# Kernel tuning notes

Hardware: AMD Instinct MI355X
Metric: run time of the kernel (lower is better)

The kernel has to match this reference:

```python
import jax, jax.numpy as jnp
import numpy as np


def conv2d(x, w, b, pad):
    y = jax.lax.conv_general_dilated(x, w, (1, 1), [(pad, pad), (pad, pad)],
                                     dimension_numbers=('NCHW', 'OIHW', 'NCHW'))
    return y + b[None, :, None, None]


def setup_inputs() -> dict:
    key = jax.random.key(0)
    ks = jax.random.split(key, 24)
    bs, C, OC, K = 2, 64, 3, 3
    hi = wi = 96
    ho = wo = 192

    def _w(k, o, i, kh, kw):
        return jax.random.normal(k, (o, i, kh, kw), jnp.float32) / np.float32(np.sqrt(i * kh * kw))

    inp = {
        'x': jax.random.normal(ks[0], (bs, C, hi, wi), jnp.float32),
        'poseMap': jax.random.normal(ks[1], (1, 3, ho, wo), jnp.float32),
        'interMapY': jax.random.randint(ks[2], (ho, wo), 0, hi, jnp.int32),
        'interMapX': jax.random.randint(ks[3], (ho, wo), 0, wi, jnp.int32),
        # sigmaconv: 3x3 convs 64->64->64->2
        'sig_w1': _w(ks[4], 64, 64, 3, 3), 'sig_b1': jnp.zeros((64,), jnp.float32),
        'sig_w2': _w(ks[5], 64, 64, 3, 3), 'sig_b2': jnp.zeros((64,), jnp.float32),
        'sig_w3': _w(ks[6], 2, 64, 3, 3), 'sig_b3': jnp.zeros((2,), jnp.float32),
        # dwconv: 1x1 convs 3->64->256->C*K*K
        'dw_w1': _w(ks[7], 64, 3, 1, 1), 'dw_b1': jnp.zeros((64,), jnp.float32),
        'dw_w2': _w(ks[8], 256, 64, 1, 1), 'dw_b2': jnp.zeros((256,), jnp.float32),
        'dw_w3': _w(ks[9], C * K * K, 256, 1, 1), 'dw_b3': jnp.zeros((C * K * K,), jnp.float32),
        # pwconv: 1x1 convs 3->64->256->C*OC
        'pw_w1': _w(ks[10], 64, 3, 1, 1), 'pw_b1': jnp.zeros((64,), jnp.float32),
        'pw_w2': _w(ks[11], 256, 64, 1, 1), 'pw_b2': jnp.zeros((256,), jnp.float32),
        'pw_w3': _w(ks[12], C * OC, 256, 1, 1), 'pw_b3': jnp.zeros((C * OC,), jnp.float32),
    }
    return inp


def reference(x, poseMap, interMapY, interMapX,
              sig_w1, sig_b1, sig_w2, sig_b2, sig_w3, sig_b3,
              dw_w1, dw_b1, dw_w2, dw_b2, dw_w3, dw_b3,
              pw_w1, pw_b1, pw_w2, pw_b2, pw_w3, pw_b3):
    C, K, OC = 64, 3, 3
    bs, _, hi, wi = x.shape
    ho, wo = poseMap.shape[2], poseMap.shape[3]
    pad = K // 2

    p = jax.lax.stop_gradient(poseMap)  # original detaches poseMap
    # kernel-predict branches (1x1 conv MLPs over position map)
    dw = conv2d(jax.nn.relu(conv2d(jax.nn.relu(conv2d(p, dw_w1, dw_b1, 0)), dw_w2, dw_b2, 0)), dw_w3, dw_b3, 0)
    dw = dw.reshape(1, C, K * K, ho, wo)
    pw = conv2d(jax.nn.relu(conv2d(jax.nn.relu(conv2d(p, pw_w1, pw_b1, 0)), pw_w2, pw_b2, 0)), pw_w3, pw_b3, 0)
    pw = pw.reshape(C, OC, ho, wo)

    # unfold(x, K, padding=K//2): [bs, C, K*K, hi, wi], kernel taps row-major
    xp = jnp.pad(x, ((0, 0), (0, 0), (pad, pad), (pad, pad)))
    h = jnp.stack([xp[:, :, dy:dy + hi, dx:dx + wi]
                   for dy in range(K) for dx in range(K)], axis=2)
    # irregular spatial gather to HR grid: [bs, C, K*K, ho, wo]
    h = h[:, :, :, interMapY, interMapX]

    mean = jnp.sum(h * jax.nn.softmax(dw, axis=2), axis=2)  # [bs, C, ho, wo]
    sigma = conv2d(jax.nn.relu(conv2d(jax.nn.relu(conv2d(mean, sig_w1, sig_b1, 1)), sig_w2, sig_b2, 1)), sig_w3, sig_b3, 1)
    sigmad = sigma[:, 0:1, None, :, :]
    sigmar = sigma[:, 1:2, None, :, :]
    bw = sigmad * dw + sigmar * jnp.abs(h - mean[:, :, None, :, :])
    xa = jnp.sum(h * jax.nn.softmax(bw, axis=2), axis=2)  # [bs, C, ho, wo]
    out = jnp.einsum('bchw,cohw->bohw', xa, pw)  # [bs, OC, ho, wo]
    return out
```

## Files before the change

kernel.cpp:

```cpp
#include <hip/hip_runtime.h>
#include <hip/hip_bf16.h>

#define NPIX 36864

typedef __attribute__((ext_vector_type(8))) short short8;
typedef __attribute__((ext_vector_type(4))) short short4v;
typedef __attribute__((ext_vector_type(4))) float float4v;

__device__ inline unsigned short f2b(float x) {
    return __builtin_bit_cast(unsigned short, __float2bfloat16(x));
}
__device__ inline float b2f(unsigned short h) {
    return __uint_as_float(((unsigned int)h) << 16);
}

#define WB_TOTAL 312320
#define XCAST_N  1179648
__global__ __launch_bounds__(256) void prep_all(
    const float* __restrict__ dw2, const float* __restrict__ dw3,
    const float* __restrict__ pw2, const float* __restrict__ pw3,
    const float* __restrict__ sw1, const float* __restrict__ sw2,
    const float* __restrict__ sw3, unsigned short* __restrict__ wb,
    const float* __restrict__ x, unsigned short* __restrict__ xb)
{
    int i = blockIdx.x * 256 + threadIdx.x;
    if (i >= WB_TOTAL) {
        int j = i - WB_TOTAL;
        if (j < XCAST_N) xb[j] = f2b(x[j]);
        return;
    }
    unsigned short v;
    if (i < 16384)        v = f2b(dw2[i]);
    else if (i < 32768)   v = f2b(pw2[i - 16384]);
    else if (i < 180224)  v = f2b(dw3[i - 32768]);
    else if (i < 229376)  v = f2b(pw3[i - 180224]);
    else if (i < 266240) { int j = i - 229376; int t = j / 4096, r = j % 4096, oc = r / 64, ic = r % 64;
                           v = f2b(sw1[(oc * 64 + ic) * 9 + t]); }
    else if (i < 303104) { int j = i - 266240; int t = j / 4096, r = j % 4096, oc = r / 64, ic = r % 64;
                           v = f2b(sw2[(oc * 64 + ic) * 9 + t]); }
    else                 { int j = i - 303104; int t = j / 1024, r = j % 1024, oc = r / 64, ic = r % 64;
                           v = (oc < 2) ? f2b(sw3[(oc * 64 + ic) * 9 + t]) : (unsigned short)0; }
    wb[i] = v;
}

__global__ __launch_bounds__(256) void mlp_fused(
    const float* __restrict__ pose,
    const float* __restrict__ w1A, const float* __restrict__ b1A,
    const float* __restrict__ w1B, const float* __restrict__ b1B,
    const unsigned short* __restrict__ w2A, const unsigned short* __restrict__ w2B,
    const float* __restrict__ b2A, const float* __restrict__ b2B,
    const unsigned short* __restrict__ w33,
    const float* __restrict__ b3A, const float* __restrict__ b3B,
    unsigned short* __restrict__ outA, unsigned short* __restrict__ outB)
{
    __shared__ unsigned short sh[16384 + 4096];
    unsigned short* h2s = sh;
    unsigned short* Ts  = sh;
    unsigned short* h1s = sh + 16384;
    const int tid = threadIdx.x;
    const int u = blockIdx.y;
    const int chain = (u == 3) ? 1 : 0;
    const int px0 = blockIdx.x * 64;
    const int w = tid >> 6, l = tid & 63;
    const int ln = l & 15, lkg = l >> 4, lk = lkg * 8;
    const float* w1 = chain ? w1B : w1A;
    const float* b1 = chain ? b1B : b1A;
    const unsigned short* w2 = chain ? w2B : w2A;
    const float* b2 = chain ? b2B : b2A;
    {
        int px = px0 + l;
        float p0 = pose[px], p1 = pose[NPIX + px], p2 = pose[2 * NPIX + px];
        short8 s0, s1;
        #pragma unroll
        for (int j = 0; j < 16; ++j) {
            int oc = w * 16 + j;
            float v = b1[oc] + w1[oc * 3] * p0 + w1[oc * 3 + 1] * p1 + w1[oc * 3 + 2] * p2;
            unsigned short uv = f2b(fmaxf(v, 0.f));
            if (j < 8) s0[j] = (short)uv; else s1[j - 8] = (short)uv;
        }
        *(short8*)&h1s[(w * 2 + 0) * 512 + l * 8] = s0;
        *(short8*)&h1s[(w * 2 + 1) * 512 + l * 8] = s1;
    }
    __syncthreads();
    {
        short8 b0v[4], b1v[4];
        #pragma unroll
        for (int nt = 0; nt < 4; ++nt) {
            b0v[nt] = *(const short8*)&h1s[(lkg    ) * 512 + (nt * 16 + ln) * 8];
            b1v[nt] = *(const short8*)&h1s[(4 + lkg) * 512 + (nt * 16 + ln) * 8];
        }
        float4v acc[4][4] = {};
        #pragma unroll
        for (int mt = 0; mt < 4; ++mt) {
            int ocr = w * 64 + mt * 16 + ln;
            short8 a0 = *(const short8*)&w2[(size_t)ocr * 64 + lk];
            short8 a1 = *(const short8*)&w2[(size_t)ocr * 64 + 32 + lk];
            #pragma unroll
            for (int nt = 0; nt < 4; ++nt) {
                acc[mt][nt] = __builtin_amdgcn_mfma_f32_16x16x32_bf16(a0, b0v[nt], acc[mt][nt], 0, 0, 0);
                acc[mt][nt] = __builtin_amdgcn_mfma_f32_16x16x32_bf16(a1, b1v[nt], acc[mt][nt], 0, 0, 0);
            }
        }
        #pragma unroll
        for (int mt = 0; mt < 4; ++mt) {
            int ocb = w * 64 + mt * 16 + lkg * 4;
            int chk = ocb >> 3, pos = (lkg & 1) * 4;
            float bv0 = b2[ocb + 0], bv1 = b2[ocb + 1], bv2 = b2[ocb + 2], bv3 = b2[ocb + 3];
            #pragma unroll
            for (int nt = 0; nt < 4; ++nt) {
                int pxl = nt * 16 + ln;
                short4v pk;
                pk[0] = (short)f2b(fmaxf(acc[mt][nt][0] + bv0, 0.f));
                pk[1] = (short)f2b(fmaxf(acc[mt][nt][1] + bv1, 0.f));
                pk[2] = (short)f2b(fmaxf(acc[mt][nt][2] + bv2, 0.f));
                pk[3] = (short)f2b(fmaxf(acc[mt][nt][3] + bv3, 0.f));
                *(short4v*)&h2s[chk * 512 + pxl * 8 + pos] = pk;
            }
        }
    }
    __syncthreads();
    const int rowbase = chain ? 576 : u * 192;
    const int obase   = chain ? 0 : u * 192;
    const float* b3 = chain ? b3B : b3A;
    unsigned short* outp = chain ? outB : outA;
    float4v acc[3][4] = {};
    const int r0 = rowbase + w * 48 + ln;
    #pragma unroll
    for (int kc = 0; kc < 8; ++kc) {
        short8 a0 = *(const short8*)&w33[(size_t)(r0 +  0) * 256 + kc * 32 + lk];
        short8 a1 = *(const short8*)&w33[(size_t)(r0 + 16) * 256 + kc * 32 + lk];
        short8 a2 = *(const short8*)&w33[(size_t)(r0 + 32) * 256 + kc * 32 + lk];
        #pragma unroll
        for (int nt = 0; nt < 4; ++nt) {
            short8 b = *(const short8*)&h2s[(kc * 4 + lkg) * 512 + (nt * 16 + ln) * 8];
            acc[0][nt] = __builtin_amdgcn_mfma_f32_16x16x32_bf16(a0, b, acc[0][nt], 0, 0, 0);
            acc[1][nt] = __builtin_amdgcn_mfma_f32_16x16x32_bf16(a1, b, acc[1][nt], 0, 0, 0);
            acc[2][nt] = __builtin_amdgcn_mfma_f32_16x16x32_bf16(a2, b, acc[2][nt], 0, 0, 0);
        }
    }
    __syncthreads();
    #pragma unroll
    for (int mt = 0; mt < 3; ++mt) {
        const int tr = w * 48 + mt * 16 + lkg * 4;
        #pragma unroll
        for (int r = 0; r < 4; ++r) {
            float bv = b3[obase + tr + r];
            #pragma unroll
            for (int nt = 0; nt < 4; ++nt)
                Ts[(tr + r) * 72 + nt * 16 + ln] = f2b(acc[mt][nt][r] + bv);
        }
    }
    __syncthreads();
    for (int i = tid; i < 1536; i += 256) {
        int row = i >> 3, pc = (i & 7) * 8;
        *(short8*)&outp[(size_t)(obase + row) * NPIX + px0 + pc] = *(const short8*)&Ts[row * 72 + pc];
    }
}

template<int MT>
__global__ __launch_bounds__(256) void conv3x3_mfma(
    const unsigned short* __restrict__ act, const unsigned short* __restrict__ wgt,
    const float* __restrict__ bias, unsigned short* __restrict__ out,
    int relu)
{
    constexpr int SP = 72;
    constexpr int OCP = MT * 16;
    __shared__ unsigned short Bs[4 * 66 * SP];
    const int tid = threadIdx.x;
    int bx = blockIdx.x;
    const int xt = bx % 3; bx /= 3;
    const int yg = bx % 96; const int b = bx / 96;
    const int y0 = yg * 2;
    const int x0 = xt * 64;
    const size_t actb = (size_t)b * NPIX * 64;
    const int w = tid >> 6, l = tid & 63;
    const int ln = l & 15, lkg = l >> 4, lk = lkg * 8;
    const int mt = (MT == 4) ? w : 0;
    short8 Wr[9][2];
    #pragma unroll
    for (int t = 0; t < 9; ++t)
        #pragma unroll
        for (int hh = 0; hh < 2; ++hh)
            Wr[t][hh] = *(const short8*)&wgt[((size_t)t * OCP + mt * 16 + ln) * 64 + hh * 32 + lk];
    for (int s = tid; s < 264; s += 256) {
        int r = s / 66, i = s % 66;
        int yy = y0 + r - 1, xx = x0 + i - 1;
        unsigned short* dst = &Bs[(r * 66 + i) * SP];
        if (yy >= 0 && yy < 192 && xx >= 0 && xx < 192) {
            const unsigned short* src = &act[actb + (size_t)(yy * 192 + xx) * 64];
            #pragma unroll
            for (int j = 0; j < 8; ++j) *(short8*)(dst + j * 8) = *(const short8*)(src + j * 8);
        } else {
            short8 z = {};
            #pragma unroll
            for (int j = 0; j < 8; ++j) *(short8*)(dst + j * 8) = z;
        }
    }
    __syncthreads();
    const int NT = (MT == 4) ? 4 : 1;
    const int ntb = (MT == 4) ? 0 : w;
    float4v acc[2][4] = {};
    #pragma unroll
    for (int t = 0; t < 9; ++t) {
        const int r = t / 3, dx = t % 3;
        #pragma unroll
        for (int hh = 0; hh < 2; ++hh) {
            #pragma unroll
            for (int o = 0; o < 2; ++o) {
                #pragma unroll
                for (int n = 0; n < 4; ++n) {
                    if (n >= NT) break;
                    int slot = (o + r) * 66 + (ntb + n) * 16 + ln + dx;
                    short8 bf = *(const short8*)&Bs[slot * SP + hh * 32 + lk];
                    acc[o][n] = __builtin_amdgcn_mfma_f32_16x16x32_bf16(Wr[t][hh], bf, acc[o][n], 0, 0, 0);
                }
            }
        }
    }
    #pragma unroll
    for (int o = 0; o < 2; ++o) {
        #pragma unroll
        for (int n = 0; n < 4; ++n) {
            if (n >= NT) break;
            int px = (y0 + o) * 192 + x0 + (ntb + n) * 16 + ln;
            if (MT == 4) {
                int oc = mt * 16 + lkg * 4;
                float v0 = acc[o][n][0] + bias[oc + 0];
                float v1 = acc[o][n][1] + bias[oc + 1];
                float v2 = acc[o][n][2] + bias[oc + 2];
                float v3 = acc[o][n][3] + bias[oc + 3];
                if (relu) { v0 = fmaxf(v0, 0.f); v1 = fmaxf(v1, 0.f); v2 = fmaxf(v2, 0.f); v3 = fmaxf(v3, 0.f); }
                uint2 pk;
                pk.x = (unsigned int)f2b(v0) | (((unsigned int)f2b(v1)) << 16);
                pk.y = (unsigned int)f2b(v2) | (((unsigned int)f2b(v3)) << 16);
                *(uint2*)&out[((size_t)b * NPIX + px) * 64 + oc] = pk;
            } else if (lkg == 0) {
                float v0 = acc[o][n][0] + bias[0];
                float v1 = acc[o][n][1] + bias[1];
                out[((size_t)b * 2 + 0) * NPIX + px] = f2b(v0);
                out[((size_t)b * 2 + 1) * NPIX + px] = f2b(v1);
            }
        }
    }
}

#define PLSZ 10192
__global__ __launch_bounds__(256) void mean_k(
    const unsigned short* __restrict__ xb, const int* __restrict__ imy, const int* __restrict__ imx,
    const unsigned short* __restrict__ dw, unsigned short* __restrict__ mean_cm)
{
    __shared__ unsigned short pl[PLSZ];
    const int c = blockIdx.y;
    const int px0 = blockIdx.x * 1024;
    const int tid = threadIdx.x;
    {
        short8 z = {};
        short8* pf = (short8*)pl;
        for (int i = tid; i < PLSZ / 8; i += 256) pf[i] = z;
    }
    float wk[4][9];
    int base[4];
    #pragma unroll
    for (int q = 0; q < 4; ++q) {
        int px = px0 + q * 256 + tid;
        base[q] = imy[px] * 104 + imx[px] + 3;
        float d[9];
        #pragma unroll
        for (int k = 0; k < 9; ++k) d[k] = b2f(dw[(size_t)(c * 9 + k) * NPIX + px]);
        float m = d[0];
        #pragma unroll
        for (int k = 1; k < 9; ++k) m = fmaxf(m, d[k]);
        float s = 0.f;
        #pragma unroll
        for (int k = 0; k < 9; ++k) { wk[q][k] = __expf(d[k] - m); s += wk[q][k]; }
        float inv = 1.f / s;
        #pragma unroll
        for (int k = 0; k < 9; ++k) wk[q][k] *= inv;
    }
    #pragma unroll
    for (int b = 0; b < 2; ++b) {
        __syncthreads();
        const unsigned short* xp = xb + (size_t)(b * 64 + c) * 9216;
        for (int i = tid; i < 96 * 12; i += 256) {
            int row = i / 12, ch = i % 12;
            const short4v* src = (const short4v*)&xp[row * 96 + ch * 8];
            unsigned short* dd = &pl[(row + 1) * 104 + 4 + ch * 8];
            *(short4v*)dd = src[0];
            *(short4v*)(dd + 4) = src[1];
        }
        __syncthreads();
        #pragma unroll
        for (int q = 0; q < 4; ++q) {
            int px = px0 + q * 256 + tid;
            float a = 0.f;
            #pragma unroll
            for (int k = 0; k < 9; ++k)
                a += wk[q][k] * b2f(pl[base[q] + (k / 3) * 104 + (k % 3)]);
            mean_cm[(size_t)(b * 64 + c) * NPIX + px] = f2b(a);
        }
    }
}

__global__ __launch_bounds__(256) void tr_k(
    const unsigned short* __restrict__ in, unsigned short* __restrict__ out)
{
    __shared__ unsigned short T[64 * 68];
    int px0 = blockIdx.x * 64;
    int b = blockIdx.y;
    int tid = threadIdx.x;
    for (int i = tid; i < 4096; i += 256) {
        int c = i >> 6, p = i & 63;
        T[p * 68 + c] = in[(size_t)(b * 64 + c) * NPIX + px0 + p];
    }
    __syncthreads();
    for (int i = tid; i < 4096; i += 256) {
        int p = i >> 6, c = i & 63;
        out[((size_t)b * NPIX + px0 + p) * 64 + c] = T[p * 68 + c];
    }
}

__global__ __launch_bounds__(256) void xa_k(
    const unsigned short* __restrict__ xb, const int* __restrict__ imy, const int* __restrict__ imx,
    const unsigned short* __restrict__ dw, const unsigned short* __restrict__ mean_cm,
    const unsigned short* __restrict__ sigma, unsigned short* __restrict__ xab)
{
    __shared__ unsigned short pl[PLSZ];
    const int c = blockIdx.y;
    const int px0 = blockIdx.x * 1024;
    const int tid = threadIdx.x;
    {
        short8 z = {};
        short8* pf = (short8*)pl;
        for (int i = tid; i < PLSZ / 8; i += 256) pf[i] = z;
    }
    float d[4][9];
    int base[4];
    #pragma unroll
    for (int q = 0; q < 4; ++q) {
        int px = px0 + q * 256 + tid;
        base[q] = imy[px] * 104 + imx[px] + 3;
        #pragma unroll
        for (int k = 0; k < 9; ++k) d[q][k] = b2f(dw[(size_t)(c * 9 + k) * NPIX + px]);
    }
    #pragma unroll
    for (int b = 0; b < 2; ++b) {
        __syncthreads();
        const unsigned short* xp = xb + (size_t)(b * 64 + c) * 9216;
        for (int i = tid; i < 96 * 12; i += 256) {
            int row = i / 12, ch = i % 12;
            const short4v* src = (const short4v*)&xp[row * 96 + ch * 8];
            unsigned short* dd = &pl[(row + 1) * 104 + 4 + ch * 8];
            *(short4v*)dd = src[0];
            *(short4v*)(dd + 4) = src[1];
        }
        __syncthreads();
        #pragma unroll
        for (int q = 0; q < 4; ++q) {
            int px = px0 + q * 256 + tid;
            float mn = b2f(mean_cm[(size_t)(b * 64 + c) * NPIX + px]);
            float sd = b2f(sigma[((size_t)b * 2 + 0) * NPIX + px]);
            float sr = b2f(sigma[((size_t)b * 2 + 1) * NPIX + px]);
            float h[9], bw[9];
            #pragma unroll
            for (int k = 0; k < 9; ++k) {
                h[k] = b2f(pl[base[q] + (k / 3) * 104 + (k % 3)]);
                bw[k] = sd * d[q][k] + sr * fabsf(h[k] - mn);
            }
            float m = bw[0];
            #pragma unroll
            for (int k = 1; k < 9; ++k) m = fmaxf(m, bw[k]);
            float s = 0.f, a = 0.f;
            #pragma unroll
            for (int k = 0; k < 9; ++k) { float e = __expf(bw[k] - m); s += e; a += e * h[k]; }
            xab[(size_t)(b * 64 + c) * NPIX + px] = f2b(a / s);
        }
    }
}

__global__ __launch_bounds__(256) void einsum_k(
    const unsigned short* __restrict__ xab, const unsigned short* __restrict__ pw,
    float* __restrict__ out)
{
    __shared__ float red[3][4][64];
    const int tid = threadIdx.x;
    const int pxl = tid & 63, cq = tid >> 6;
    const int px = blockIdx.x * 64 + pxl;
    const int b = blockIdx.y;
    float a0 = 0.f, a1 = 0.f, a2 = 0.f;
    #pragma unroll
    for (int ci = 0; ci < 16; ++ci) {
        int c = cq * 16 + ci;
        float v = b2f(xab[(size_t)(b * 64 + c) * NPIX + px]);
        a0 += v * b2f(pw[(size_t)(c * 3 + 0) * NPIX + px]);
        a1 += v * b2f(pw[(size_t)(c * 3 + 1) * NPIX + px]);
        a2 += v * b2f(pw[(size_t)(c * 3 + 2) * NPIX + px]);
    }
    red[0][cq][pxl] = a0;
    red[1][cq][pxl] = a1;
    red[2][cq][pxl] = a2;
    __syncthreads();
    if (cq < 3) {
        float s = red[cq][0][pxl] + red[cq][1][pxl] + red[cq][2][pxl] + red[cq][3][pxl];
        out[((size_t)b * 3 + cq) * NPIX + px] = s;
    }
}

extern "C" void kernel_launch(void* const* d_in, const int* in_sizes, int n_in,
                              void* d_out, int out_size, void* d_ws, size_t ws_size,
                              hipStream_t stream)
{
    (void)in_sizes; (void)n_in; (void)out_size; (void)ws_size;
    const float* x      = (const float*)d_in[0];
    const float* pose   = (const float*)d_in[1];
    const int*   imy    = (const int*)d_in[2];
    const int*   imx    = (const int*)d_in[3];
    const float* sig_w1 = (const float*)d_in[4];
    const float* sig_b1 = (const float*)d_in[5];
    const float* sig_w2 = (const float*)d_in[6];
    const float* sig_b2 = (const float*)d_in[7];
    const float* sig_w3 = (const float*)d_in[8];
    const float* sig_b3 = (const float*)d_in[9];
    const float* dw_w1  = (const float*)d_in[10];
    const float* dw_b1  = (const float*)d_in[11];
    const float* dw_w2  = (const float*)d_in[12];
    const float* dw_b2  = (const float*)d_in[13];
    const float* dw_w3  = (const float*)d_in[14];
    const float* dw_b3  = (const float*)d_in[15];
    const float* pw_w1  = (const float*)d_in[16];
    const float* pw_b1  = (const float*)d_in[17];
    const float* pw_w2  = (const float*)d_in[18];
    const float* pw_b2  = (const float*)d_in[19];
    const float* pw_w3  = (const float*)d_in[20];
    const float* pw_b3  = (const float*)d_in[21];
    float* out = (float*)d_out;

    unsigned short* ws = (unsigned short*)d_ws;
    size_t off = 0;
    unsigned short* wb      = ws + off; off += WB_TOTAL;
    unsigned short* xb16    = ws + off; off += (size_t)XCAST_N;
    unsigned short* dwbuf   = ws + off; off += (size_t)576 * NPIX;
    unsigned short* pwbuf   = ws + off; off += (size_t)192 * NPIX;
    unsigned short* mean_cm = ws + off; off += (size_t)2 * 64 * NPIX;
    unsigned short* mean_pm = ws + off; off += (size_t)2 * NPIX * 64;
    unsigned short* s1      = ws + off; off += (size_t)2 * NPIX * 64;
    unsigned short* s2      = ws + off; off += (size_t)2 * NPIX * 64;
    unsigned short* sigma   = ws + off; off += (size_t)2 * 2 * NPIX;
    unsigned short* xab     = ws + off; off += (size_t)2 * 64 * NPIX;

    unsigned short* w_dw2 = wb + 0;
    unsigned short* w_pw2 = wb + 16384;
    unsigned short* w_33  = wb + 32768;
    unsigned short* w_s1t = wb + 229376;
    unsigned short* w_s2t = wb + 266240;
    unsigned short* w_s3t = wb + 303104;

    dim3 blk(256);
    prep_all<<<dim3((WB_TOTAL + XCAST_N + 255) / 256), blk, 0, stream>>>(
        dw_w2, dw_w3, pw_w2, pw_w3, sig_w1, sig_w2, sig_w3, wb, x, xb16);
    mlp_fused<<<dim3(576, 4), blk, 0, stream>>>(
        pose, dw_w1, dw_b1, pw_w1, pw_b1, w_dw2, w_pw2, dw_b2, pw_b2,
        w_33, dw_b3, pw_b3, dwbuf, pwbuf);
    mean_k<<<dim3(36, 64), blk, 0, stream>>>(xb16, imy, imx, dwbuf, mean_cm);
    tr_k<<<dim3(576, 2), blk, 0, stream>>>(mean_cm, mean_pm);
    conv3x3_mfma<4><<<dim3(576), blk, 0, stream>>>(mean_pm, w_s1t, sig_b1, s1, 1);
    conv3x3_mfma<4><<<dim3(576), blk, 0, stream>>>(s1,      w_s2t, sig_b2, s2, 1);
    conv3x3_mfma<1><<<dim3(576), blk, 0, stream>>>(s2,      w_s3t, sig_b3, sigma, 0);
    xa_k<<<dim3(36, 64), blk, 0, stream>>>(xb16, imy, imx, dwbuf, mean_cm, sigma, xab);
    einsum_k<<<dim3(576, 2), blk, 0, stream>>>(xab, pwbuf, out);
}
```

Measured before the change: 252.0 us.

## Make mlp_fused persistent over pixel tiles with register-resident weight fragments

The MLP kernel now launches 128x4 blocks instead of 576x4. Each block loops over 4-5 pixel tiles and loads its layer-2 and layer-3 bf16 weight fragments into registers once, so they are not re-read for every tile. Layer-2 accumulation is restructured to produce and store each 16x16 tile right away, and launch bounds request 2 blocks per CU. The cost is much higher register pressure (24 short8 for Aw3 plus 8 for Aw2) and fewer blocks, which could lower occupancy or cause spills.

```diff
diff --git a/kernel.cpp b/kernel.cpp
--- a/kernel.cpp
+++ b/kernel.cpp
@@ -43,7 +43,7 @@
     wb[i] = v;
 }
 
-__global__ __launch_bounds__(256) void mlp_fused(
+__global__ __launch_bounds__(256, 2) void mlp_fused(
     const float* __restrict__ pose,
     const float* __restrict__ w1A, const float* __restrict__ b1A,
     const float* __restrict__ w1B, const float* __restrict__ b1B,
@@ -60,100 +60,110 @@
     const int tid = threadIdx.x;
     const int u = blockIdx.y;
     const int chain = (u == 3) ? 1 : 0;
-    const int px0 = blockIdx.x * 64;
     const int w = tid >> 6, l = tid & 63;
     const int ln = l & 15, lkg = l >> 4, lk = lkg * 8;
     const float* w1 = chain ? w1B : w1A;
     const float* b1 = chain ? b1B : b1A;
     const unsigned short* w2 = chain ? w2B : w2A;
     const float* b2 = chain ? b2B : b2A;
-    {
-        int px = px0 + l;
-        float p0 = pose[px], p1 = pose[NPIX + px], p2 = pose[2 * NPIX + px];
-        short8 s0, s1;
-        #pragma unroll
-        for (int j = 0; j < 16; ++j) {
-            int oc = w * 16 + j;
-            float v = b1[oc] + w1[oc * 3] * p0 + w1[oc * 3 + 1] * p1 + w1[oc * 3 + 2] * p2;
-            unsigned short uv = f2b(fmaxf(v, 0.f));
-            if (j < 8) s0[j] = (short)uv; else s1[j - 8] = (short)uv;
-        }
-        *(short8*)&h1s[(w * 2 + 0) * 512 + l * 8] = s0;
-        *(short8*)&h1s[(w * 2 + 1) * 512 + l * 8] = s1;
-    }
-    __syncthreads();
-    {
-        short8 b0v[4], b1v[4];
-        #pragma unroll
-        for (int nt = 0; nt < 4; ++nt) {
-            b0v[nt] = *(const short8*)&h1s[(lkg    ) * 512 + (nt * 16 + ln) * 8];
-            b1v[nt] = *(const short8*)&h1s[(4 + lkg) * 512 + (nt * 16 + ln) * 8];
-        }
-        float4v acc[4][4] = {};
-        #pragma unroll
-        for (int mt = 0; mt < 4; ++mt) {
-            int ocr = w * 64 + mt * 16 + ln;
-            short8 a0 = *(const short8*)&w2[(size_t)ocr * 64 + lk];
-            short8 a1 = *(const short8*)&w2[(size_t)ocr * 64 + 32 + lk];
-            #pragma unroll
-            for (int nt = 0; nt < 4; ++nt) {
-                acc[mt][nt] = __builtin_amdgcn_mfma_f32_16x16x32_bf16(a0, b0v[nt], acc[mt][nt], 0, 0, 0);
-                acc[mt][nt] = __builtin_amdgcn_mfma_f32_16x16x32_bf16(a1, b1v[nt], acc[mt][nt], 0, 0, 0);
-            }
-        }
-        #pragma unroll
-        for (int mt = 0; mt < 4; ++mt) {
-            int ocb = w * 64 + mt * 16 + lkg * 4;
-            int chk = ocb >> 3, pos = (lkg & 1) * 4;
-            float bv0 = b2[ocb + 0], bv1 = b2[ocb + 1], bv2 = b2[ocb + 2], bv3 = b2[ocb + 3];
-            #pragma unroll
-            for (int nt = 0; nt < 4; ++nt) {
-                int pxl = nt * 16 + ln;
-                short4v pk;
-                pk[0] = (short)f2b(fmaxf(acc[mt][nt][0] + bv0, 0.f));
-                pk[1] = (short)f2b(fmaxf(acc[mt][nt][1] + bv1, 0.f));
-                pk[2] = (short)f2b(fmaxf(acc[mt][nt][2] + bv2, 0.f));
-                pk[3] = (short)f2b(fmaxf(acc[mt][nt][3] + bv3, 0.f));
-                *(short4v*)&h2s[chk * 512 + pxl * 8 + pos] = pk;
-            }
-        }
-    }
-    __syncthreads();
     const int rowbase = chain ? 576 : u * 192;
     const int obase   = chain ? 0 : u * 192;
     const float* b3 = chain ? b3B : b3A;
     unsigned short* outp = chain ? outB : outA;
-    float4v acc[3][4] = {};
+
+    short8 Aw2[4][2];
+    #pragma unroll
+    for (int mt = 0; mt < 4; ++mt) {
+        int ocr = w * 64 + mt * 16 + ln;
+        Aw2[mt][0] = *(const short8*)&w2[(size_t)ocr * 64 + lk];
+        Aw2[mt][1] = *(const short8*)&w2[(size_t)ocr * 64 + 32 + lk];
+    }
     const int r0 = rowbase + w * 48 + ln;
+    short8 Aw3[3][8];
     #pragma unroll
     for (int kc = 0; kc < 8; ++kc) {
-        short8 a0 = *(const short8*)&w33[(size_t)(r0 +  0) * 256 + kc * 32 + lk];
-        short8 a1 = *(const short8*)&w33[(size_t)(r0 + 16) * 256 + kc * 32 + lk];
-        short8 a2 = *(const short8*)&w33[(size_t)(r0 + 32) * 256 + kc * 32 + lk];
-        #pragma unroll
-        for (int nt = 0; nt < 4; ++nt) {
-            short8 b = *(const short8*)&h2s[(kc * 4 + lkg) * 512 + (nt * 16 + ln) * 8];
-            acc[0][nt] = __builtin_amdgcn_mfma_f32_16x16x32_bf16(a0, b, acc[0][nt], 0, 0, 0);
-            acc[1][nt] = __builtin_amdgcn_mfma_f32_16x16x32_bf16(a1, b, acc[1][nt], 0, 0, 0);
-            acc[2][nt] = __builtin_amdgcn_mfma_f32_16x16x32_bf16(a2, b, acc[2][nt], 0, 0, 0);
-        }
-    }
-    __syncthreads();
-    #pragma unroll
-    for (int mt = 0; mt < 3; ++mt) {
-        const int tr = w * 48 + mt * 16 + lkg * 4;
-        #pragma unroll
-        for (int r = 0; r < 4; ++r) {
-            float bv = b3[obase + tr + r];
-            #pragma unroll
-            for (int nt = 0; nt < 4; ++nt)
-                Ts[(tr + r) * 72 + nt * 16 + ln] = f2b(acc[mt][nt][r] + bv);
-        }
-    }
-    __syncthreads();
-    for (int i = tid; i < 1536; i += 256) {
-        int row = i >> 3, pc = (i & 7) * 8;
-        *(short8*)&outp[(size_t)(obase + row) * NPIX + px0 + pc] = *(const short8*)&Ts[row * 72 + pc];
+        Aw3[0][kc] = *(const short8*)&w33[(size_t)(r0 +  0) * 256 + kc * 32 + lk];
+        Aw3[1][kc] = *(const short8*)&w33[(size_t)(r0 + 16) * 256 + kc * 32 + lk];
+        Aw3[2][kc] = *(const short8*)&w33[(size_t)(r0 + 32) * 256 + kc * 32 + lk];
+    }
+
+    const int bx = blockIdx.x;
+    const int niter = (bx < 64) ? 5 : 4;
+    const int tbase = (bx < 64) ? bx * 5 : 320 + (bx - 64) * 4;
+
+    for (int it = 0; it < niter; ++it) {
+        const int px0 = (tbase + it) * 64;
+        {
+            int px = px0 + l;
+            float p0 = pose[px], p1 = pose[NPIX + px], p2 = pose[2 * NPIX + px];
+            short8 s0, s1;
+            #pragma unroll
+            for (int j = 0; j < 16; ++j) {
+                int oc = w * 16 + j;
+                float v = b1[oc] + w1[oc * 3] * p0 + w1[oc * 3 + 1] * p1 + w1[oc * 3 + 2] * p2;
+                unsigned short uv = f2b(fmaxf(v, 0.f));
+                if (j < 8) s0[j] = (short)uv; else s1[j - 8] = (short)uv;
+            }
+            *(short8*)&h1s[(w * 2 + 0) * 512 + l * 8] = s0;
+            *(short8*)&h1s[(w * 2 + 1) * 512 + l * 8] = s1;
+        }
+        __syncthreads();
+        {
+            short8 b0v[4], b1v[4];
+            #pragma unroll
+            for (int nt = 0; nt < 4; ++nt) {
+                b0v[nt] = *(const short8*)&h1s[(lkg    ) * 512 + (nt * 16 + ln) * 8];
+                b1v[nt] = *(const short8*)&h1s[(4 + lkg) * 512 + (nt * 16 + ln) * 8];
+            }
+            #pragma unroll
+            for (int mt = 0; mt < 4; ++mt) {
+                int ocb = w * 64 + mt * 16 + lkg * 4;
+                int chk = ocb >> 3, pos = (lkg & 1) * 4;
+                float bv0 = b2[ocb + 0], bv1 = b2[ocb + 1], bv2 = b2[ocb + 2], bv3 = b2[ocb + 3];
+                #pragma unroll
+                for (int nt = 0; nt < 4; ++nt) {
+                    float4v acc = {};
+                    acc = __builtin_amdgcn_mfma_f32_16x16x32_bf16(Aw2[mt][0], b0v[nt], acc, 0, 0, 0);
+                    acc = __builtin_amdgcn_mfma_f32_16x16x32_bf16(Aw2[mt][1], b1v[nt], acc, 0, 0, 0);
+                    int pxl = nt * 16 + ln;
+                    short4v pk;
+                    pk[0] = (short)f2b(fmaxf(acc[0] + bv0, 0.f));
+                    pk[1] = (short)f2b(fmaxf(acc[1] + bv1, 0.f));
+                    pk[2] = (short)f2b(fmaxf(acc[2] + bv2, 0.f));
+                    pk[3] = (short)f2b(fmaxf(acc[3] + bv3, 0.f));
+                    *(short4v*)&h2s[chk * 512 + pxl * 8 + pos] = pk;
+                }
+            }
+        }
+        __syncthreads();
+        float4v acc[3][4] = {};
+        #pragma unroll
+        for (int kc = 0; kc < 8; ++kc) {
+            #pragma unroll
+            for (int nt = 0; nt < 4; ++nt) {
+                short8 b = *(const short8*)&h2s[(kc * 4 + lkg) * 512 + (nt * 16 + ln) * 8];
+                acc[0][nt] = __builtin_amdgcn_mfma_f32_16x16x32_bf16(Aw3[0][kc], b, acc[0][nt], 0, 0, 0);
+                acc[1][nt] = __builtin_amdgcn_mfma_f32_16x16x32_bf16(Aw3[1][kc], b, acc[1][nt], 0, 0, 0);
+                acc[2][nt] = __builtin_amdgcn_mfma_f32_16x16x32_bf16(Aw3[2][kc], b, acc[2][nt], 0, 0, 0);
+            }
+        }
+        __syncthreads();
+        #pragma unroll
+        for (int mt = 0; mt < 3; ++mt) {
+            const int tr = w * 48 + mt * 16 + lkg * 4;
+            #pragma unroll
+            for (int r = 0; r < 4; ++r) {
+                float bv = b3[obase + tr + r];
+                #pragma unroll
+                for (int nt = 0; nt < 4; ++nt)
+                    Ts[(tr + r) * 72 + nt * 16 + ln] = f2b(acc[mt][nt][r] + bv);
+            }
+        }
+        __syncthreads();
+        for (int i = tid; i < 1536; i += 256) {
+            int row = i >> 3, pc = (i & 7) * 8;
+            *(short8*)&outp[(size_t)(obase + row) * NPIX + px0 + pc] = *(const short8*)&Ts[row * 72 + pc];
+        }
     }
 }
 
@@ -457,7 +467,7 @@
     dim3 blk(256);
     prep_all<<<dim3((WB_TOTAL + XCAST_N + 255) / 256), blk, 0, stream>>>(
         dw_w2, dw_w3, pw_w2, pw_w3, sig_w1, sig_w2, sig_w3, wb, x, xb16);
-    mlp_fused<<<dim3(576, 4), blk, 0, stream>>>(
+    mlp_fused<<<dim3(128, 4), blk, 0, stream>>>(
         pose, dw_w1, dw_b1, pw_w1, pw_b1, w_dw2, w_pw2, dw_b2, pw_b2,
         w_33, dw_b3, pw_b3, dwbuf, pwbuf);
     mean_k<<<dim3(36, 64), blk, 0, stream>>>(xb16, imy, imx, dwbuf, mean_cm);
```

After: 265.9 us. 5.5% more time.
